# Optimization experiments

Hardware: AMD Instinct MI355X
Metric: run time of the kernel (lower is better)

## Reference

```python
import jax, jax.numpy as jnp
import numpy as np

N, E, D, G, L = 100_000, 500_000, 128, 512, 4
BN_EPS = 1e-5

def _bn(v, g, b):
    # BatchNorm1d in training mode: biased batch stats over node/graph axis
    m = v.mean(0)
    var = v.var(0)
    return (v - m) * jax.lax.rsqrt(var + BN_EPS) * g + b

def setup_inputs() -> dict:
    key = jax.random.key(0)
    ks = jax.random.split(key, 12)
    s = 0.05
    return {
        "x": jax.random.normal(ks[0], (N, D), jnp.float32),
        "edge_index": jax.random.randint(ks[1], (2, E), 0, N, jnp.int64),
        "batch": jnp.sort(jax.random.randint(ks[2], (N,), 0, G, jnp.int64)),
        "num_graphs": G,
        "W1": jax.random.normal(ks[3], (L, D, 2 * D), jnp.float32) * s,
        "b1": jnp.zeros((L, 2 * D), jnp.float32),
        "g1": jnp.ones((L, 2 * D), jnp.float32),
        "be1": jnp.zeros((L, 2 * D), jnp.float32),
        "W2": jax.random.normal(ks[4], (L, 2 * D, D), jnp.float32) * s,
        "b2": jnp.zeros((L, D), jnp.float32),
        "gbn": jnp.ones((L, D), jnp.float32),
        "bbn": jnp.zeros((L, D), jnp.float32),
        "eps": jnp.zeros((L,), jnp.float32),
        "cW1": jax.random.normal(ks[5], (3 * D, D), jnp.float32) * s,
        "cb1": jnp.zeros((D,), jnp.float32),
        "cg": jnp.ones((D,), jnp.float32),
        "cbeta": jnp.zeros((D,), jnp.float32),
        "cW2": jax.random.normal(ks[6], (D, D // 2), jnp.float32) * s,
        "cb2": jnp.zeros((D // 2,), jnp.float32),
        "cW3": jax.random.normal(ks[7], (D // 2, 2), jnp.float32) * s,
        "cb3": jnp.zeros((2,), jnp.float32),
    }

def reference(x, edge_index, batch, num_graphs, W1, b1, g1, be1, W2, b2, gbn, bbn, eps,
              cW1, cb1, cg, cbeta, cW2, cb2, cW3, cb3):
    n = x.shape[0]
    src, dst = edge_index[0], edge_index[1]
    for l in range(W1.shape[0]):
        # GINConv: mlp((1+eps)*x + sum_{j in N(i)} x_j)  (scatter-add to dst)
        agg = jax.ops.segment_sum(x[src], dst, num_segments=n)
        h = (1.0 + eps[l]) * x + agg
        h = jax.nn.relu(_bn(h @ W1[l] + b1[l], g1[l], be1[l]))
        h = h @ W2[l] + b2[l]
        x = jax.nn.relu(_bn(h, gbn[l], bbn[l]))  # outer BN + ReLU (dropout off: eval)
    # multi-pool readout: add / mean / max per graph
    s = jax.ops.segment_sum(x, batch, num_segments=num_graphs)
    cnt = jax.ops.segment_sum(jnp.ones((n,), x.dtype), batch, num_segments=num_graphs)
    mean = s / jnp.maximum(cnt, 1.0)[:, None]
    mx = jax.ops.segment_max(x, batch, num_segments=num_graphs)
    z = jnp.concatenate([s, mean, mx], axis=-1)  # [G, 3*D]
    z = jax.nn.relu(_bn(z @ cW1 + cb1, cg, cbeta))
    z = jax.nn.relu(z @ cW2 + cb2)
    return z @ cW3 + cb3
```

## Files before the change

### kernel.cpp

```cpp
#include <hip/hip_runtime.h>
#include <cstdint>
#include <cstddef>

#define NN 100000
#define EE 500000
#define DD 128
#define GG 512
#define LL 4
#define BN_EPS 1e-5f

typedef __attribute__((ext_vector_type(8))) short short8;
typedef __attribute__((ext_vector_type(8))) unsigned short ushort8v;
typedef __attribute__((ext_vector_type(4))) float f32x4;

static __device__ __forceinline__ unsigned short f2bf(float f) {
  union { float f; unsigned u; } v;
  v.f = f;
  unsigned r = v.u + 0x7fffu + ((v.u >> 16) & 1u);
  return (unsigned short)(r >> 16);
}
static __device__ __forceinline__ float bf2f(unsigned short u) {
  union { unsigned u; float f; } v;
  v.u = ((unsigned)u) << 16;
  return v.f;
}


__global__ void k_hist(const int* __restrict__ ei, int* __restrict__ cnt) {
  int e = blockIdx.x * 256 + threadIdx.x;
  if (e < EE) {
    int d = ei[EE + e];
    if (d >= 0 && d < NN) atomicAdd(&cnt[d], 1);
  }
}

__global__ void k_part(const int* __restrict__ cnt, int* __restrict__ part) {
  __shared__ int sm[1024];
  int t = threadIdx.x;
  int i = blockIdx.x * 1024 + t;
  sm[t] = (i < NN) ? cnt[i] : 0;
  __syncthreads();
  for (int off = 512; off > 0; off >>= 1) {
    if (t < off) sm[t] += sm[t + off];
    __syncthreads();
  }
  if (t == 0) part[blockIdx.x] = sm[0];
}

__global__ void k_scanpart(const int* __restrict__ part, int* __restrict__ partx, int nb) {
  __shared__ int sm[128];
  int t = threadIdx.x;
  int v = (t < nb) ? part[t] : 0;
  sm[t] = v;
  __syncthreads();
  for (int off = 1; off < 128; off <<= 1) {
    int u = (t >= off) ? sm[t - off] : 0;
    __syncthreads();
    sm[t] += u;
    __syncthreads();
  }
  if (t < nb) partx[t] = sm[t] - v;
}

__global__ void k_rs(const int* __restrict__ cnt, const int* __restrict__ partx,
                     int* __restrict__ rs, int* __restrict__ cur) {
  __shared__ int sm[1024];
  int t = threadIdx.x;
  int i = blockIdx.x * 1024 + t;
  int v = (i < NN) ? cnt[i] : 0;
  sm[t] = v;
  __syncthreads();
  for (int off = 1; off < 1024; off <<= 1) {
    int u = (t >= off) ? sm[t - off] : 0;
    __syncthreads();
    sm[t] += u;
    __syncthreads();
  }
  if (i < NN) {
    int excl = partx[blockIdx.x] + sm[t] - v;
    rs[i] = excl;
    cur[i] = excl;
    if (i == NN - 1) rs[NN] = excl + v;
  }
}

__global__ void k_fill(const int* __restrict__ ei, int* __restrict__ cur,
                       int* __restrict__ ci) {
  int e = blockIdx.x * 256 + threadIdx.x;
  if (e < EE) {
    int s = ei[e];
    int d = ei[EE + e];
    if (d >= 0 && d < NN && s >= 0 && s < NN) {
      int pos = atomicAdd(&cur[d], 1);
      if (pos >= 0 && pos < EE) ci[pos] = s;
    }
  }
}


__global__ void k_conv(const float* __restrict__ W1, const float* __restrict__ W2,
                       unsigned short* __restrict__ W1t, unsigned short* __restrict__ W2t) {
  int idx = blockIdx.x * 256 + threadIdx.x;
  if (idx < 4 * 256 * 128) {
    {
      int l = idx >> 15, rem = idx & 32767;
      int nc = rem >> 7, k = rem & 127;
      W1t[idx] = f2bf(W1[(l << 15) + k * 256 + nc]);
    }
    {
      int l = idx >> 15, rem = idx & 32767;
      int nc = rem >> 8, k = rem & 255;
      W2t[idx] = f2bf(W2[(l << 15) + k * 128 + nc]);
    }
  }
}


__global__ void k_x2bf(const float* __restrict__ x, unsigned short* __restrict__ xb) {
  int i = blockIdx.x * 256 + threadIdx.x;
  if (i < NN * DD / 4) {
    float4 v = *(const float4*)(x + (size_t)i * 4);
    ushort4 o;
    o.x = f2bf(v.x); o.y = f2bf(v.y); o.z = f2bf(v.z); o.w = f2bf(v.w);
    *(ushort4*)(xb + (size_t)i * 4) = o;
  }
}


__global__ __launch_bounds__(256) void k_agg_bf16(
    const unsigned short* __restrict__ X, const int* __restrict__ rs,
    const int* __restrict__ ci, const float* __restrict__ epsv, int l, int mode,
    const float* __restrict__ tsc, const float* __restrict__ tsh,
    unsigned short* __restrict__ h0, int n) {
  int idx = blockIdx.x * 256 + threadIdx.x;
  int node = idx >> 4;
  int c8 = (idx & 15) << 3;
  if (node >= n) return;
  float sa[8], sb[8];
  if (mode) {
    float4 a0 = *(const float4*)(tsc + c8), a1 = *(const float4*)(tsc + c8 + 4);
    float4 b0 = *(const float4*)(tsh + c8), b1 = *(const float4*)(tsh + c8 + 4);
    sa[0] = a0.x; sa[1] = a0.y; sa[2] = a0.z; sa[3] = a0.w;
    sa[4] = a1.x; sa[5] = a1.y; sa[6] = a1.z; sa[7] = a1.w;
    sb[0] = b0.x; sb[1] = b0.y; sb[2] = b0.z; sb[3] = b0.w;
    sb[4] = b1.x; sb[5] = b1.y; sb[6] = b1.z; sb[7] = b1.w;
  }
  float se = 1.f + epsv[l];
  ushort8v v = *(const ushort8v*)(X + (size_t)node * DD + c8);
  float acc[8];
#pragma unroll
  for (int j = 0; j < 8; ++j) {
    float f = bf2f(v[j]);
    if (mode) f = fmaxf(0.f, f * sa[j] + sb[j]);
    acc[j] = se * f;
  }
  int e0 = rs[node], e1 = rs[node + 1];
  ushort8v un;
  if (e0 < e1) un = *(const ushort8v*)(X + (size_t)ci[e0] * DD + c8);
  for (int e = e0; e < e1; ++e) {
    ushort8v uc = un;
    if (e + 1 < e1) un = *(const ushort8v*)(X + (size_t)ci[e + 1] * DD + c8);
#pragma unroll
    for (int j = 0; j < 8; ++j) {
      float f = bf2f(uc[j]);
      if (mode) f = fmaxf(0.f, f * sa[j] + sb[j]);
      acc[j] += f;
    }
  }
  ushort8v o;
#pragma unroll
  for (int j = 0; j < 8; ++j) o[j] = f2bf(acc[j]);
  *(ushort8v*)(h0 + (size_t)node * DD + c8) = o;
}


template <int K, int NC>
__global__ __launch_bounds__(256) void k_gemm(
    const unsigned short* __restrict__ A, int mode, const float* __restrict__ tsc,
    const float* __restrict__ tsh, const unsigned short* __restrict__ Bt,
    const float* __restrict__ bias, unsigned short* __restrict__ C,
    float* __restrict__ psum, float* __restrict__ psq, int n) {
  constexpr int KC = 64;
  constexpr int KT = K / KC;
  constexpr int NT = NC / 128;
  constexpr int AST = 72;
  constexpr int CTP = 136;
  __shared__ __align__(16) unsigned short smem[(64 + 128) * AST];
  __shared__ float bsum[128], bsq[128];
  unsigned short* Asm = smem;
  unsigned short* Bsm = smem + 64 * AST;
  unsigned short* Ct = smem;

  int tid = threadIdx.x;
  int lane = tid & 63, wave = tid >> 6;
  int quad = lane >> 4, l15 = lane & 15;
  int row0 = blockIdx.x * 64;
  int blk = blockIdx.x;

  for (int cg = 0; cg < NT; ++cg) {
    f32x4 acc[8];
#pragma unroll
    for (int j = 0; j < 8; ++j) acc[j] = (f32x4){0.f, 0.f, 0.f, 0.f};

    for (int kc = 0; kc < KT; ++kc) {
      __syncthreads();
#pragma unroll
      for (int it = 0; it < 2; ++it) {
        int f = tid + it * 256;
        int r = f >> 3;
        int c8 = (f & 7) << 3;
        int gr = row0 + r;
        ushort8v v = (ushort8v){0, 0, 0, 0, 0, 0, 0, 0};
        if (gr < n) v = *(const ushort8v*)(A + (size_t)gr * K + kc * KC + c8);
        if (mode) {
          int kg = kc * KC + c8;
          float4 s0 = *(const float4*)(tsc + kg);
          float4 s1 = *(const float4*)(tsc + kg + 4);
          float4 t0 = *(const float4*)(tsh + kg);
          float4 t1 = *(const float4*)(tsh + kg + 4);
          float sa[8] = {s0.x, s0.y, s0.z, s0.w, s1.x, s1.y, s1.z, s1.w};
          float sb[8] = {t0.x, t0.y, t0.z, t0.w, t1.x, t1.y, t1.z, t1.w};
#pragma unroll
          for (int j = 0; j < 8; ++j)
            v[j] = f2bf(fmaxf(0.f, bf2f(v[j]) * sa[j] + sb[j]));
        }
        *(ushort8v*)(&Asm[r * AST + c8]) = v;
      }
#pragma unroll
      for (int it = 0; it < 4; ++it) {
        int f = tid + it * 256;
        int r = f >> 3;
        int c8 = (f & 7) << 3;
        *(ushort8v*)(&Bsm[r * AST + c8]) =
            *(const ushort8v*)(Bt + (size_t)(cg * 128 + r) * K + kc * KC + c8);
      }
      if (kc == 0 && tid < 128) { bsum[tid] = 0.f; bsq[tid] = 0.f; }
      __syncthreads();
#pragma unroll
      for (int kk = 0; kk < KC; kk += 32) {
        int ko = kk + quad * 8;
        short8 av = *(const short8*)(&Asm[(wave * 16 + l15) * AST + ko]);
#pragma unroll
        for (int cf = 0; cf < 8; ++cf) {
          short8 bv = *(const short8*)(&Bsm[(cf * 16 + l15) * AST + ko]);
          acc[cf] = __builtin_amdgcn_mfma_f32_16x16x32_bf16(av, bv, acc[cf], 0, 0, 0);
        }
      }
    }

    __syncthreads();
    float s8[8], q8[8];
#pragma unroll
    for (int j = 0; j < 8; ++j) { s8[j] = 0.f; q8[j] = 0.f; }
    int lrbase = wave * 16 + quad * 4;
#pragma unroll
    for (int cf = 0; cf < 8; ++cf) {
      int col = cg * 128 + cf * 16 + l15;
      float bv = bias[col];
#pragma unroll
      for (int reg = 0; reg < 4; ++reg) {
        int lr = lrbase + reg;
        float e = acc[cf][reg] + bv;
        Ct[lr * CTP + cf * 16 + l15] = f2bf(e);
        if (row0 + lr < n) { s8[cf] += e; q8[cf] += e * e; }
      }
    }
#pragma unroll
    for (int cf = 0; cf < 8; ++cf) {
      s8[cf] += __shfl_xor(s8[cf], 16, 64);
      s8[cf] += __shfl_xor(s8[cf], 32, 64);
      q8[cf] += __shfl_xor(q8[cf], 16, 64);
      q8[cf] += __shfl_xor(q8[cf], 32, 64);
    }
    __syncthreads();
    if (quad == 0) {
#pragma unroll
      for (int cf = 0; cf < 8; ++cf) {
        atomicAdd(&bsum[cf * 16 + l15], s8[cf]);
        atomicAdd(&bsq[cf * 16 + l15], q8[cf]);
      }
    }
#pragma unroll
    for (int it = 0; it < 4; ++it) {
      int f = tid + it * 256;
      int r = f >> 4;
      int c8 = (f & 15) << 3;
      int gr = row0 + r;
      if (gr < n)
        *(ushort8v*)(C + (size_t)gr * NC + cg * 128 + c8) =
            *(const ushort8v*)(&Ct[r * CTP + c8]);
    }
    __syncthreads();
    if (tid < 128) {
      psum[(size_t)blk * NC + cg * 128 + tid] = bsum[tid];
      psq[(size_t)blk * NC + cg * 128 + tid] = bsq[tid];
    }
  }
}


__global__ __launch_bounds__(256) void k_finred(
    const float* __restrict__ psum, const float* __restrict__ psq, int nb, int nc,
    const float* __restrict__ g, const float* __restrict__ be,
    float* __restrict__ osc, float* __restrict__ osh, float invn) {
  __shared__ float ws[4], wq[4];
  int col = blockIdx.x;
  int t = threadIdx.x;
  float s = 0.f, q = 0.f;
  for (int b = t; b < nb; b += 256) {
    s += psum[(size_t)b * nc + col];
    q += psq[(size_t)b * nc + col];
  }
#pragma unroll
  for (int off = 32; off > 0; off >>= 1) {
    s += __shfl_xor(s, off, 64);
    q += __shfl_xor(q, off, 64);
  }
  if ((t & 63) == 0) { ws[t >> 6] = s; wq[t >> 6] = q; }
  __syncthreads();
  if (t == 0) {
    s = ws[0] + ws[1] + ws[2] + ws[3];
    q = wq[0] + wq[1] + wq[2] + wq[3];
    float m = s * invn;
    float v = fmaxf(q * invn - m * m, 0.f);
    float sc = g[col] * rsqrtf(v + BN_EPS);
    osc[col] = sc;
    osh[col] = be[col] - m * sc;
  }
}


__global__ __launch_bounds__(256) void k_statz(
    const float* __restrict__ z1, const float* __restrict__ g,
    const float* __restrict__ be, float* __restrict__ osc, float* __restrict__ osh) {
  __shared__ float ws[4], wq[4];
  int col = blockIdx.x;
  int t = threadIdx.x;
  float s = 0.f, q = 0.f;
  for (int b = t; b < GG; b += 256) {
    float v = z1[(size_t)b * 128 + col];
    s += v;
    q += v * v;
  }
#pragma unroll
  for (int off = 32; off > 0; off >>= 1) {
    s += __shfl_xor(s, off, 64);
    q += __shfl_xor(q, off, 64);
  }
  if ((t & 63) == 0) { ws[t >> 6] = s; wq[t >> 6] = q; }
  __syncthreads();
  if (t == 0) {
    s = ws[0] + ws[1] + ws[2] + ws[3];
    q = wq[0] + wq[1] + wq[2] + wq[3];
    float m = s / (float)GG;
    float v = fmaxf(q / (float)GG - m * m, 0.f);
    float sc = g[col] * rsqrtf(v + BN_EPS);
    osc[col] = sc;
    osh[col] = be[col] - m * sc;
  }
}


static __device__ __forceinline__ int lb_i32(const int* a, int n, int key) {
  int lo = 0, hi = n;
  while (lo < hi) {
    int mid = (lo + hi) >> 1;
    if (a[mid] < key) lo = mid + 1; else hi = mid;
  }
  return lo;
}

__global__ __launch_bounds__(512) void k_pool(
    const unsigned short* __restrict__ X, const int* __restrict__ batch,
    const float* __restrict__ tsc, const float* __restrict__ tsh,
    float* __restrict__ z, int n) {
  __shared__ int slo, shi;
  __shared__ float ssum[8][128], smax[8][128];
  int g = blockIdx.x;
  int t = threadIdx.x;
  int sg = t >> 6;
  int c2 = (t & 63) << 1;
  if (t == 0) {
    slo = lb_i32(batch, n, g);
    shi = lb_i32(batch, n, g + 1);
  }
  __syncthreads();
  int lo = slo, hi = shi;
  float a0 = tsc[c2], a1 = tsc[c2 + 1];
  float b0 = tsh[c2], b1 = tsh[c2 + 1];
  float s0 = 0.f, s1 = 0.f;
  float m0 = -3.402823466e38f, m1 = -3.402823466e38f;
  for (int i = lo + sg; i < hi; i += 8) {
    unsigned u = *(const unsigned*)(X + (size_t)i * DD + c2);
    float v0 = fmaxf(0.f, bf2f((unsigned short)(u & 0xffff)) * a0 + b0);
    float v1 = fmaxf(0.f, bf2f((unsigned short)(u >> 16)) * a1 + b1);
    s0 += v0; m0 = fmaxf(m0, v0);
    s1 += v1; m1 = fmaxf(m1, v1);
  }
  ssum[sg][c2] = s0; ssum[sg][c2 + 1] = s1;
  smax[sg][c2] = m0; smax[sg][c2 + 1] = m1;
  __syncthreads();
  if (t < 128) {
    float S = 0.f, M = -3.402823466e38f;
#pragma unroll
    for (int k = 0; k < 8; ++k) {
      S += ssum[k][t];
      M = fmaxf(M, smax[k][t]);
    }
    float cntf = (float)(hi - lo);
    z[(size_t)g * 384 + t] = S;
    z[(size_t)g * 384 + 128 + t] = S / fmaxf(cntf, 1.f);
    z[(size_t)g * 384 + 256 + t] = M;
  }
}


__global__ void k_cls1(const float* __restrict__ z, const float* __restrict__ cW1,
                       const float* __restrict__ cb1, float* __restrict__ z1) {
  __shared__ float zr[384];
  int g = blockIdx.x;
  int c = threadIdx.x;
  for (int i = c; i < 384; i += 128) zr[i] = z[(size_t)g * 384 + i];
  __syncthreads();
  float s = cb1[c];
#pragma unroll 4
  for (int k = 0; k < 384; ++k) s = fmaf(zr[k], cW1[(size_t)k * 128 + c], s);
  z1[(size_t)g * 128 + c] = s;
}

__global__ void k_cls2(const float* __restrict__ z1, const float* __restrict__ csc,
                       const float* __restrict__ csh, const float* __restrict__ cW2,
                       const float* __restrict__ cb2, const float* __restrict__ cW3,
                       const float* __restrict__ cb3, float* __restrict__ out) {
  __shared__ float z1n[128];
  __shared__ float z2s[64];
  int g = blockIdx.x;
  int t = threadIdx.x;
  z1n[t] = fmaxf(0.f, z1[(size_t)g * 128 + t] * csc[t] + csh[t]);
  __syncthreads();
  if (t < 64) {
    float s = cb2[t];
#pragma unroll 4
    for (int k = 0; k < 128; ++k) s = fmaf(z1n[k], cW2[(size_t)k * 64 + t], s);
    z2s[t] = fmaxf(0.f, s);
  }
  __syncthreads();
  if (t < 2) {
    float s = cb3[t];
#pragma unroll 4
    for (int c = 0; c < 64; ++c) s = fmaf(z2s[c], cW3[(size_t)c * 2 + t], s);
    out[(size_t)g * 2 + t] = s;
  }
}


extern "C" void kernel_launch(void* const* d_in, const int* in_sizes, int n_in,
                              void* d_out, int out_size, void* d_ws, size_t ws_size,
                              hipStream_t stream) {
  const float* x = (const float*)d_in[0];
  const int* ei = (const int*)d_in[1];
  const int* batch = (const int*)d_in[2];
  const float* W1 = (const float*)d_in[4];
  const float* b1 = (const float*)d_in[5];
  const float* g1 = (const float*)d_in[6];
  const float* be1 = (const float*)d_in[7];
  const float* W2 = (const float*)d_in[8];
  const float* b2 = (const float*)d_in[9];
  const float* gbn = (const float*)d_in[10];
  const float* bbn = (const float*)d_in[11];
  const float* epsv = (const float*)d_in[12];
  const float* cW1 = (const float*)d_in[13];
  const float* cb1 = (const float*)d_in[14];
  const float* cg = (const float*)d_in[15];
  const float* cbeta = (const float*)d_in[16];
  const float* cW2 = (const float*)d_in[17];
  const float* cb2 = (const float*)d_in[18];
  const float* cW3 = (const float*)d_in[19];
  const float* cb3 = (const float*)d_in[20];
  float* out = (float*)d_out;

  char* p = (char*)d_ws;
  auto alloc = [&](size_t bytes) {
    char* r = p;
    p += (bytes + 255) & ~(size_t)255;
    return r;
  };
  const int NB = (NN + 63) / 64;
  int* cnt = (int*)alloc((size_t)NN * 4);
  int* rs = (int*)alloc((size_t)(NN + 1) * 4);
  int* cur = (int*)alloc((size_t)NN * 4);
  int* ci = (int*)alloc((size_t)EE * 4);
  int* part = (int*)alloc(128 * 4);
  int* partx = (int*)alloc(128 * 4);
  unsigned short* xbf = (unsigned short*)alloc((size_t)NN * DD * 2);
  unsigned short* h0 = (unsigned short*)alloc((size_t)NN * DD * 2);
  unsigned short* h1 = (unsigned short*)alloc((size_t)NN * 2 * DD * 2);
  unsigned short* xp = (unsigned short*)alloc((size_t)NN * DD * 2);
  float* psum = (float*)alloc((size_t)NB * 256 * 4);
  float* psq = (float*)alloc((size_t)NB * 256 * 4);
  float* tsc1 = (float*)alloc(256 * 4);
  float* tsh1 = (float*)alloc(256 * 4);
  float* tscX = (float*)alloc(128 * 4);
  float* tshX = (float*)alloc(128 * 4);
  float* zbuf = (float*)alloc((size_t)GG * 384 * 4);
  float* z1 = (float*)alloc((size_t)GG * 128 * 4);
  unsigned short* W1t = (unsigned short*)alloc((size_t)4 * 256 * 128 * 2);
  unsigned short* W2t = (unsigned short*)alloc((size_t)4 * 128 * 256 * 2);
  (void)ws_size; (void)n_in; (void)in_sizes; (void)out_size;

  k_conv<<<512, 256, 0, stream>>>(W1, W2, W1t, W2t);
  k_x2bf<<<(NN * DD / 4 + 255) / 256, 256, 0, stream>>>(x, xbf);

  hipMemsetAsync(cnt, 0, (size_t)NN * 4, stream);
  k_hist<<<(EE + 255) / 256, 256, 0, stream>>>(ei, cnt);
  const int nscan = (NN + 1023) / 1024;
  k_part<<<nscan, 1024, 0, stream>>>(cnt, part);
  k_scanpart<<<1, 128, 0, stream>>>(part, partx, nscan);
  k_rs<<<nscan, 1024, 0, stream>>>(cnt, partx, rs, cur);
  k_fill<<<(EE + 255) / 256, 256, 0, stream>>>(ei, cur, ci);

  for (int l = 0; l < LL; ++l) {
    const unsigned short* Xl = (l == 0) ? xbf : xp;
    k_agg_bf16<<<(NN * 16 + 255) / 256, 256, 0, stream>>>(
        Xl, rs, ci, epsv, l, (l > 0) ? 1 : 0, tscX, tshX, h0, NN);
    k_gemm<128, 256><<<NB, 256, 0, stream>>>(
        h0, 0, nullptr, nullptr, W1t + (size_t)l * 256 * 128,
        b1 + (size_t)l * 256, h1, psum, psq, NN);
    k_finred<<<256, 256, 0, stream>>>(psum, psq, NB, 256, g1 + (size_t)l * 256,
                                      be1 + (size_t)l * 256, tsc1, tsh1, 1.0f / NN);
    k_gemm<256, 128><<<NB, 256, 0, stream>>>(
        h1, 1, tsc1, tsh1, W2t + (size_t)l * 128 * 256,
        b2 + (size_t)l * 128, xp, psum, psq, NN);
    k_finred<<<128, 256, 0, stream>>>(psum, psq, NB, 128, gbn + (size_t)l * 128,
                                      bbn + (size_t)l * 128, tscX, tshX, 1.0f / NN);
  }

  k_pool<<<GG, 512, 0, stream>>>(xp, batch, tscX, tshX, zbuf, NN);
  k_cls1<<<GG, 128, 0, stream>>>(zbuf, cW1, cb1, z1);
  k_statz<<<128, 256, 0, stream>>>(z1, cg, cbeta, tscX, tshX);
  k_cls2<<<GG, 128, 0, stream>>>(z1, tscX, tshX, cW2, cb2, cW3, cb3, out);
}
```

Baseline: 789.2 us.

## Enlarge GEMM tile to 128 rows and register-prefetch next K chunk

The fused GEMM+BN-stats kernel now uses 512 threads and 128-row tiles instead of 256 threads and 64 rows, which halves the block count and the per-block partial-stat rows. The column-group and K-chunk loops are flattened into one loop, and the next chunk's A and B tiles are loaded into registers while the MFMAs for the current chunk run. This hides global-load latency behind compute at the cost of more registers per thread and a larger shared-memory footprint, which may lower occupancy. The B tile is still reloaded for every block.

```diff
diff --git a/kernel.cpp b/kernel.cpp
--- a/kernel.cpp
+++ b/kernel.cpp
@@ -175,7 +175,7 @@
 
 
 template <int K, int NC>
-__global__ __launch_bounds__(256) void k_gemm(
+__global__ __launch_bounds__(512) void k_gemm(
     const unsigned short* __restrict__ A, int mode, const float* __restrict__ tsc,
     const float* __restrict__ tsh, const unsigned short* __restrict__ Bt,
     const float* __restrict__ bias, unsigned short* __restrict__ C,
@@ -183,117 +183,136 @@
   constexpr int KC = 64;
   constexpr int KT = K / KC;
   constexpr int NT = NC / 128;
+  constexpr int P = KT * NT;
   constexpr int AST = 72;
   constexpr int CTP = 136;
-  __shared__ __align__(16) unsigned short smem[(64 + 128) * AST];
+  __shared__ __align__(16) unsigned short smem[2 * 128 * AST];
   __shared__ float bsum[128], bsq[128];
   unsigned short* Asm = smem;
-  unsigned short* Bsm = smem + 64 * AST;
+  unsigned short* Bsm = smem + 128 * AST;
   unsigned short* Ct = smem;
 
   int tid = threadIdx.x;
   int lane = tid & 63, wave = tid >> 6;
   int quad = lane >> 4, l15 = lane & 15;
-  int row0 = blockIdx.x * 64;
+  int row0 = blockIdx.x * 128;
   int blk = blockIdx.x;
 
-  for (int cg = 0; cg < NT; ++cg) {
-    f32x4 acc[8];
-#pragma unroll
-    for (int j = 0; j < 8; ++j) acc[j] = (f32x4){0.f, 0.f, 0.f, 0.f};
-
-    for (int kc = 0; kc < KT; ++kc) {
-      __syncthreads();
+  ushort8v pa[2], pb[2];
+#pragma unroll
+  for (int it = 0; it < 2; ++it) {
+    int f = tid + it * 512;
+    int r = f >> 3;
+    int c8 = (f & 7) << 3;
+    int gr = row0 + r;
+    pa[it] = (ushort8v){0, 0, 0, 0, 0, 0, 0, 0};
+    if (gr < n) pa[it] = *(const ushort8v*)(A + (size_t)gr * K + c8);
+    pb[it] = *(const ushort8v*)(Bt + (size_t)r * K + c8);
+  }
+
+  f32x4 acc[8];
+  for (int p = 0; p < P; ++p) {
+    int cg = p / KT, kc = p % KT;
+    if (kc == 0) {
+#pragma unroll
+      for (int j = 0; j < 8; ++j) acc[j] = (f32x4){0.f, 0.f, 0.f, 0.f};
+    }
+#pragma unroll
+    for (int it = 0; it < 2; ++it) {
+      int f = tid + it * 512;
+      int r = f >> 3;
+      int c8 = (f & 7) << 3;
+      ushort8v v = pa[it];
+      if (mode) {
+        int kg = kc * KC + c8;
+        float4 s0 = *(const float4*)(tsc + kg);
+        float4 s1 = *(const float4*)(tsc + kg + 4);
+        float4 t0 = *(const float4*)(tsh + kg);
+        float4 t1 = *(const float4*)(tsh + kg + 4);
+        float sa[8] = {s0.x, s0.y, s0.z, s0.w, s1.x, s1.y, s1.z, s1.w};
+        float sb[8] = {t0.x, t0.y, t0.z, t0.w, t1.x, t1.y, t1.z, t1.w};
+#pragma unroll
+        for (int j = 0; j < 8; ++j)
+          v[j] = f2bf(fmaxf(0.f, bf2f(v[j]) * sa[j] + sb[j]));
+      }
+      *(ushort8v*)(&Asm[r * AST + c8]) = v;
+      *(ushort8v*)(&Bsm[r * AST + c8]) = pb[it];
+    }
+    __syncthreads();
+    if (p + 1 < P) {
+      int cg2 = (p + 1) / KT, kc2 = (p + 1) % KT;
 #pragma unroll
       for (int it = 0; it < 2; ++it) {
-        int f = tid + it * 256;
+        int f = tid + it * 512;
         int r = f >> 3;
         int c8 = (f & 7) << 3;
         int gr = row0 + r;
-        ushort8v v = (ushort8v){0, 0, 0, 0, 0, 0, 0, 0};
-        if (gr < n) v = *(const ushort8v*)(A + (size_t)gr * K + kc * KC + c8);
-        if (mode) {
-          int kg = kc * KC + c8;
-          float4 s0 = *(const float4*)(tsc + kg);
-          float4 s1 = *(const float4*)(tsc + kg + 4);
-          float4 t0 = *(const float4*)(tsh + kg);
-          float4 t1 = *(const float4*)(tsh + kg + 4);
-          float sa[8] = {s0.x, s0.y, s0.z, s0.w, s1.x, s1.y, s1.z, s1.w};
-          float sb[8] = {t0.x, t0.y, t0.z, t0.w, t1.x, t1.y, t1.z, t1.w};
-#pragma unroll
-          for (int j = 0; j < 8; ++j)
-            v[j] = f2bf(fmaxf(0.f, bf2f(v[j]) * sa[j] + sb[j]));
+        pa[it] = (ushort8v){0, 0, 0, 0, 0, 0, 0, 0};
+        if (gr < n) pa[it] = *(const ushort8v*)(A + (size_t)gr * K + kc2 * KC + c8);
+        pb[it] = *(const ushort8v*)(Bt + (size_t)(cg2 * 128 + r) * K + kc2 * KC + c8);
+      }
+    }
+#pragma unroll
+    for (int kk = 0; kk < KC; kk += 32) {
+      int ko = kk + quad * 8;
+      short8 av = *(const short8*)(&Asm[(wave * 16 + l15) * AST + ko]);
+#pragma unroll
+      for (int cf = 0; cf < 8; ++cf) {
+        short8 bv = *(const short8*)(&Bsm[(cf * 16 + l15) * AST + ko]);
+        acc[cf] = __builtin_amdgcn_mfma_f32_16x16x32_bf16(av, bv, acc[cf], 0, 0, 0);
+      }
+    }
+    if (kc == KT - 1) {
+      __syncthreads();
+      if (tid < 128) { bsum[tid] = 0.f; bsq[tid] = 0.f; }
+      float s8[8], q8[8];
+#pragma unroll
+      for (int j = 0; j < 8; ++j) { s8[j] = 0.f; q8[j] = 0.f; }
+      int lrbase = wave * 16 + quad * 4;
+#pragma unroll
+      for (int cf = 0; cf < 8; ++cf) {
+        int col = cg * 128 + cf * 16 + l15;
+        float bv = bias[col];
+#pragma unroll
+        for (int reg = 0; reg < 4; ++reg) {
+          int lr = lrbase + reg;
+          float e = acc[cf][reg] + bv;
+          Ct[lr * CTP + cf * 16 + l15] = f2bf(e);
+          if (row0 + lr < n) { s8[cf] += e; q8[cf] += e * e; }
         }
-        *(ushort8v*)(&Asm[r * AST + c8]) = v;
+      }
+#pragma unroll
+      for (int cf = 0; cf < 8; ++cf) {
+        s8[cf] += __shfl_xor(s8[cf], 16, 64);
+        s8[cf] += __shfl_xor(s8[cf], 32, 64);
+        q8[cf] += __shfl_xor(q8[cf], 16, 64);
+        q8[cf] += __shfl_xor(q8[cf], 32, 64);
+      }
+      __syncthreads();
+      if (quad == 0) {
+#pragma unroll
+        for (int cf = 0; cf < 8; ++cf) {
+          atomicAdd(&bsum[cf * 16 + l15], s8[cf]);
+          atomicAdd(&bsq[cf * 16 + l15], q8[cf]);
+        }
       }
 #pragma unroll
       for (int it = 0; it < 4; ++it) {
-        int f = tid + it * 256;
-        int r = f >> 3;
-        int c8 = (f & 7) << 3;
-        *(ushort8v*)(&Bsm[r * AST + c8]) =
-            *(const ushort8v*)(Bt + (size_t)(cg * 128 + r) * K + kc * KC + c8);
-      }
-      if (kc == 0 && tid < 128) { bsum[tid] = 0.f; bsq[tid] = 0.f; }
+        int f = tid + it * 512;
+        int r = f >> 4;
+        int c8 = (f & 15) << 3;
+        int gr = row0 + r;
+        if (gr < n)
+          *(ushort8v*)(C + (size_t)gr * NC + cg * 128 + c8) =
+              *(const ushort8v*)(&Ct[r * CTP + c8]);
+      }
       __syncthreads();
-#pragma unroll
-      for (int kk = 0; kk < KC; kk += 32) {
-        int ko = kk + quad * 8;
-        short8 av = *(const short8*)(&Asm[(wave * 16 + l15) * AST + ko]);
-#pragma unroll
-        for (int cf = 0; cf < 8; ++cf) {
-          short8 bv = *(const short8*)(&Bsm[(cf * 16 + l15) * AST + ko]);
-          acc[cf] = __builtin_amdgcn_mfma_f32_16x16x32_bf16(av, bv, acc[cf], 0, 0, 0);
-        }
-      }
-    }
-
-    __syncthreads();
-    float s8[8], q8[8];
-#pragma unroll
-    for (int j = 0; j < 8; ++j) { s8[j] = 0.f; q8[j] = 0.f; }
-    int lrbase = wave * 16 + quad * 4;
-#pragma unroll
-    for (int cf = 0; cf < 8; ++cf) {
-      int col = cg * 128 + cf * 16 + l15;
-      float bv = bias[col];
-#pragma unroll
-      for (int reg = 0; reg < 4; ++reg) {
-        int lr = lrbase + reg;
-        float e = acc[cf][reg] + bv;
-        Ct[lr * CTP + cf * 16 + l15] = f2bf(e);
-        if (row0 + lr < n) { s8[cf] += e; q8[cf] += e * e; }
-      }
-    }
-#pragma unroll
-    for (int cf = 0; cf < 8; ++cf) {
-      s8[cf] += __shfl_xor(s8[cf], 16, 64);
-      s8[cf] += __shfl_xor(s8[cf], 32, 64);
-      q8[cf] += __shfl_xor(q8[cf], 16, 64);
-      q8[cf] += __shfl_xor(q8[cf], 32, 64);
-    }
-    __syncthreads();
-    if (quad == 0) {
-#pragma unroll
-      for (int cf = 0; cf < 8; ++cf) {
-        atomicAdd(&bsum[cf * 16 + l15], s8[cf]);
-        atomicAdd(&bsq[cf * 16 + l15], q8[cf]);
-      }
-    }
-#pragma unroll
-    for (int it = 0; it < 4; ++it) {
-      int f = tid + it * 256;
-      int r = f >> 4;
-      int c8 = (f & 15) << 3;
-      int gr = row0 + r;
-      if (gr < n)
-        *(ushort8v*)(C + (size_t)gr * NC + cg * 128 + c8) =
-            *(const ushort8v*)(&Ct[r * CTP + c8]);
-    }
-    __syncthreads();
-    if (tid < 128) {
-      psum[(size_t)blk * NC + cg * 128 + tid] = bsum[tid];
-      psq[(size_t)blk * NC + cg * 128 + tid] = bsq[tid];
+      if (tid < 128) {
+        psum[(size_t)blk * NC + cg * 128 + tid] = bsum[tid];
+        psq[(size_t)blk * NC + cg * 128 + tid] = bsq[tid];
+      }
+    } else {
+      __syncthreads();
     }
   }
 }
@@ -485,7 +504,7 @@
     p += (bytes + 255) & ~(size_t)255;
     return r;
   };
-  const int NB = (NN + 63) / 64;
+  const int NB = (NN + 127) / 128;
   int* cnt = (int*)alloc((size_t)NN * 4);
   int* rs = (int*)alloc((size_t)(NN + 1) * 4);
   int* cur = (int*)alloc((size_t)NN * 4);
@@ -523,12 +542,12 @@
     const unsigned short* Xl = (l == 0) ? xbf : xp;
     k_agg_bf16<<<(NN * 16 + 255) / 256, 256, 0, stream>>>(
         Xl, rs, ci, epsv, l, (l > 0) ? 1 : 0, tscX, tshX, h0, NN);
-    k_gemm<128, 256><<<NB, 256, 0, stream>>>(
+    k_gemm<128, 256><<<NB, 512, 0, stream>>>(
         h0, 0, nullptr, nullptr, W1t + (size_t)l * 256 * 128,
         b1 + (size_t)l * 256, h1, psum, psq, NN);
     k_finred<<<256, 256, 0, stream>>>(psum, psq, NB, 256, g1 + (size_t)l * 256,
                                       be1 + (size_t)l * 256, tsc1, tsh1, 1.0f / NN);
-    k_gemm<256, 128><<<NB, 256, 0, stream>>>(
+    k_gemm<256, 128><<<NB, 512, 0, stream>>>(
         h1, 1, tsc1, tsh1, W2t + (size_t)l * 128 * 256,
         b2 + (size_t)l * 128, xp, psum, psq, NN);
     k_finred<<<128, 256, 0, stream>>>(psum, psq, NB, 128, gbn + (size_t)l * 128,
```

After: 764.8 us. 1.03x faster.
